# Optimization experiments

Hardware: AMD Instinct MI355X
Metric: run time of the kernel (lower is better)

Reference implementation:

```python
import jax, jax.numpy as jnp
import numpy as np

N_NODES = 100000
N_EDGES = 1600000
IN_C = 64
HID_C = 64
OUT_C = 8


def _glorot(key, shape):
    fan_in, fan_out = shape
    lim = (6.0 / (fan_in + fan_out)) ** 0.5
    return jax.random.uniform(key, shape, jnp.float32, -lim, lim)


def setup_inputs() -> dict:
    key = jax.random.key(0)
    ks = jax.random.split(key, 16)
    inp = {
        "x": jax.random.normal(ks[0], (N_NODES, IN_C), jnp.float32),
        "edge_index": jax.random.randint(ks[1], (2, N_EDGES), 0, N_NODES, jnp.int64),
        "edge_attr": jax.random.normal(ks[2], (N_EDGES, 1), jnp.float32),
        # GIN MLP params: layer i uses Linear(in,h) -> ReLU -> Linear(h,h)
        "l0_w1": _glorot(ks[3], (IN_C, HID_C)), "l0_b1": jnp.zeros((HID_C,), jnp.float32),
        "l0_w2": _glorot(ks[4], (HID_C, HID_C)), "l0_b2": jnp.zeros((HID_C,), jnp.float32),
        "l1_w1": _glorot(ks[5], (HID_C, HID_C)), "l1_b1": jnp.zeros((HID_C,), jnp.float32),
        "l1_w2": _glorot(ks[6], (HID_C, HID_C)), "l1_b2": jnp.zeros((HID_C,), jnp.float32),
        # last layer maps hidden -> out (reduce_dims is None)
        "l2_w1": _glorot(ks[7], (HID_C, OUT_C)), "l2_b1": jnp.zeros((OUT_C,), jnp.float32),
        "l2_w2": _glorot(ks[8], (OUT_C, OUT_C)), "l2_b2": jnp.zeros((OUT_C,), jnp.float32),
    }
    return inp


def _gin_layer(x, src, dst, w1, b1, w2, b2):
    # GINConv with eps=0: out_i = MLP(x_i + sum_{j->i} x_j)
    agg = jax.ops.segment_sum(x[src], dst, num_segments=N_NODES)  # [N, C]
    h = x + agg
    h = jax.nn.relu(h @ w1 + b1)
    return h @ w2 + b2


def reference(x, edge_index, edge_attr,
              l0_w1, l0_b1, l0_w2, l0_b2,
              l1_w1, l1_b1, l1_w2, l1_b2,
              l2_w1, l2_b1, l2_w2, l2_b2):
    src, dst = edge_index[0], edge_index[1]
    # dropout is identity in eval mode
    h = _gin_layer(x, src, dst, l0_w1, l0_b1, l0_w2, l0_b2)
    h = jax.nn.relu(h)
    h = _gin_layer(h, src, dst, l1_w1, l1_b1, l1_w2, l1_b2)
    h = jax.nn.relu(h)
    h = _gin_layer(h, src, dst, l2_w1, l2_b1, l2_w2, l2_b2)  # no relu on last (reduce_dims None)
    return jax.nn.log_softmax(h, axis=-1)
```

## Files before the change

### kernel.cpp

```cpp
#include <hip/hip_runtime.h>
#include <math.h>

#define N_NODES 100000
#define N_EDGES 1600000
#define C 64
#define OUTC 8
#define NBUCK 256
#define BRANGE 391
#define BCAP 7200
#define CNT_PAD 64
#define BUCK_CHUNK 4096

__device__ __forceinline__ float bflo(unsigned u) { return __uint_as_float(u << 16); }
__device__ __forceinline__ float bfhi(unsigned u) { return __uint_as_float(u & 0xFFFF0000u); }
__device__ __forceinline__ unsigned short f2bf(float f) {
    unsigned b = __float_as_uint(f);
    b += 0x7FFFu + ((b >> 16) & 1u);
    return (unsigned short)(b >> 16);
}

__global__ __launch_bounds__(256) void bucket_k(const int* __restrict__ src, const int* __restrict__ dst,
                                                int* cntp, uint2* __restrict__ ebuf, int ne) {
    __shared__ int lcnt[NBUCK], lbase[NBUCK], lcur[NBUCK];
    int t = threadIdx.x;
    if (t < NBUCK) { lcnt[t] = 0; lcur[t] = 0; }
    __syncthreads();
    int base = blockIdx.x * BUCK_CHUNK;
#pragma unroll
    for (int i = 0; i < BUCK_CHUNK / 256; i++) {
        int e = base + i * 256 + t;
        if (e < ne) {
            int d = __builtin_nontemporal_load(dst + e);
            atomicAdd(&lcnt[d / BRANGE], 1);
        }
    }
    __syncthreads();
    if (t < NBUCK) lbase[t] = lcnt[t] ? atomicAdd(&cntp[t * CNT_PAD], lcnt[t]) : 0;
    __syncthreads();
#pragma unroll
    for (int i = 0; i < BUCK_CHUNK / 256; i++) {
        int e = base + i * 256 + t;
        if (e < ne) {
            int d = __builtin_nontemporal_load(dst + e);
            int s = __builtin_nontemporal_load(src + e);
            int r = d / BRANGE;
            int pos = lbase[r] + atomicAdd(&lcur[r], 1);
            if (pos < BCAP) ebuf[(size_t)r * BCAP + pos] = make_uint2((unsigned)s, (unsigned)d);
        }
    }
}

__global__ __launch_bounds__(512) void fill4_k(const int* __restrict__ cntp, const uint2* __restrict__ ebuf,
                                               int* __restrict__ rowptr, int* __restrict__ ssrc) {
    __shared__ int lcnt[BRANGE];
    __shared__ int sm[512];
    __shared__ int lcur[BRANGE];
    __shared__ int cbuf[NBUCK];
    __shared__ int bbase;
    int b = blockIdx.x;
    int lo = b * BRANGE;
    int span = N_NODES - lo; if (span > BRANGE) span = BRANGE; if (span < 0) span = 0;
    int t = threadIdx.x;
    if (t < BRANGE) lcnt[t] = 0;
    if (t < NBUCK) cbuf[t] = cntp[t * CNT_PAD];
    __syncthreads();
    if (t == 0) {
        int s = 0;
        for (int i = 0; i < b; i++) s += cbuf[i];
        bbase = s;
    }
    int cnt = cbuf[b];
    if (cnt > BCAP) cnt = BCAP;
    const uint2* buf = ebuf + (size_t)b * BCAP;
    for (int i = t; i < cnt; i += 512) {
        uint2 ed = buf[i];
        atomicAdd(&lcnt[(int)ed.y - lo], 1);
    }
    __syncthreads();
    int v = (t < BRANGE) ? lcnt[t] : 0;
    sm[t] = v;
    __syncthreads();
    for (int off = 1; off < 512; off <<= 1) {
        int u = (t >= off) ? sm[t - off] : 0;
        __syncthreads();
        sm[t] += u;
        __syncthreads();
    }
    int ex = bbase + sm[t] - v;
    if (t < span) { rowptr[lo + t] = ex; lcur[t] = ex; }
    if (b == NBUCK - 1 && t == 0) rowptr[N_NODES] = N_EDGES;
    __syncthreads();
    for (int i = t; i < cnt; i += 512) {
        uint2 ed = buf[i];
        int p = atomicAdd(&lcur[(int)ed.y - lo], 1);
        ssrc[p] = (int)ed.x;
    }
}

__global__ __launch_bounds__(256) void conv_bf16_k(const float* __restrict__ in, unsigned short* __restrict__ outb, int nElem) {
    int i = blockIdx.x * 256 + threadIdx.x;
    int stride = gridDim.x * 256;
    for (int e = i * 4; e < nElem; e += stride * 4) {
        float4 v = *(const float4*)(in + e);
        ushort4 o;
        o.x = f2bf(v.x); o.y = f2bf(v.y); o.z = f2bf(v.z); o.w = f2bf(v.w);
        *(ushort4*)(outb + e) = o;
    }
}

__global__ __launch_bounds__(256) void gather_bf16_k(const unsigned short* __restrict__ featb,
                                                     const int* __restrict__ rowptr,
                                                     const int* __restrict__ ssrc,
                                                     float* __restrict__ tout, int n) {
    const uint2* feat2 = (const uint2*)featb;
    int lane = threadIdx.x & 63;
    int slot = lane >> 4;
    int chg  = lane & 15;
    int wid = blockIdx.x * 4 + (threadIdx.x >> 6);
    if (wid >= n) return;
    int beg = rowptr[wid], end = rowptr[wid + 1];
    float ax = 0.f, ay = 0.f, az = 0.f, aw = 0.f;
    if (slot == 0) {
        uint2 v = feat2[(size_t)wid * 16 + chg];
        ax = bflo(v.x); ay = bfhi(v.x); az = bflo(v.y); aw = bfhi(v.y);
    }
    int e = beg;
    for (; e + 8 <= end; e += 8) {
        int iA = ssrc[e + slot];
        int iB = ssrc[e + 4 + slot];
        uint2 vA = feat2[(size_t)iA * 16 + chg];
        uint2 vB = feat2[(size_t)iB * 16 + chg];
        ax += bflo(vA.x) + bflo(vB.x);
        ay += bfhi(vA.x) + bfhi(vB.x);
        az += bflo(vA.y) + bflo(vB.y);
        aw += bfhi(vA.y) + bfhi(vB.y);
    }
    for (; e < end; e += 4) {
        int myE = e + slot;
        if (myE < end) {
            int i = ssrc[myE];
            uint2 v = feat2[(size_t)i * 16 + chg];
            ax += bflo(v.x); ay += bfhi(v.x); az += bflo(v.y); aw += bfhi(v.y);
        }
    }
    ax += __shfl_xor(ax, 16, 64); ay += __shfl_xor(ay, 16, 64);
    az += __shfl_xor(az, 16, 64); aw += __shfl_xor(aw, 16, 64);
    ax += __shfl_xor(ax, 32, 64); ay += __shfl_xor(ay, 32, 64);
    az += __shfl_xor(az, 32, 64); aw += __shfl_xor(aw, 32, 64);
    if (slot == 0) ((float4*)tout)[(size_t)wid * 16 + chg] = make_float4(ax, ay, az, aw);
}

__global__ __launch_bounds__(256) void fused_final_bf16_k(const unsigned short* __restrict__ featb,
                                                          const int* __restrict__ rowptr,
                                                          const int* __restrict__ ssrc,
                                                          float* __restrict__ out,
                                                          const float* __restrict__ W1, const float* __restrict__ b1,
                                                          const float* __restrict__ W2, const float* __restrict__ b2,
                                                          int n) {
    const uint2* feat2 = (const uint2*)featb;
    int lane = threadIdx.x & 63;
    int slot = lane >> 4;
    int chg  = lane & 15;
    int j = lane & 7;
    int g = lane >> 3;
    float w1r[8], w2r[8];
#pragma unroll
    for (int i = 0; i < 8; i++) w1r[i] = W1[(g * 8 + i) * OUTC + j];
#pragma unroll
    for (int i = 0; i < 8; i++) w2r[i] = W2[i * OUTC + j];
    float b1j = b1[j], b2j = b2[j];
    int wid = blockIdx.x * 4 + (threadIdx.x >> 6);
    if (wid >= n) return;
    int beg = rowptr[wid], end = rowptr[wid + 1];
    float ax = 0.f, ay = 0.f, az = 0.f, aw = 0.f;
    if (slot == 0) {
        uint2 v = feat2[(size_t)wid * 16 + chg];
        ax = bflo(v.x); ay = bfhi(v.x); az = bflo(v.y); aw = bfhi(v.y);
    }
    int e = beg;
    for (; e + 8 <= end; e += 8) {
        int iA = ssrc[e + slot];
        int iB = ssrc[e + 4 + slot];
        uint2 vA = feat2[(size_t)iA * 16 + chg];
        uint2 vB = feat2[(size_t)iB * 16 + chg];
        ax += bflo(vA.x) + bflo(vB.x);
        ay += bfhi(vA.x) + bfhi(vB.x);
        az += bflo(vA.y) + bflo(vB.y);
        aw += bfhi(vA.y) + bfhi(vB.y);
    }
    for (; e < end; e += 4) {
        int myE = e + slot;
        if (myE < end) {
            int i = ssrc[myE];
            uint2 v = feat2[(size_t)i * 16 + chg];
            ax += bflo(v.x); ay += bfhi(v.x); az += bflo(v.y); aw += bfhi(v.y);
        }
    }
    ax += __shfl_xor(ax, 16, 64); ay += __shfl_xor(ay, 16, 64);
    az += __shfl_xor(az, 16, 64); aw += __shfl_xor(aw, 16, 64);
    ax += __shfl_xor(ax, 32, 64); ay += __shfl_xor(ay, 32, 64);
    az += __shfl_xor(az, 32, 64); aw += __shfl_xor(aw, 32, 64);
    float h = 0.f;
#pragma unroll
    for (int i = 0; i < 8; i++) {
        float compv = (i & 3) == 0 ? ax : (i & 3) == 1 ? ay : (i & 3) == 2 ? az : aw;
        float tm = __shfl(compv, g * 2 + (i >> 2), 64);
        h = fmaf(tm, w1r[i], h);
    }
    h += __shfl_xor(h, 8, 64);
    h += __shfl_xor(h, 16, 64);
    h += __shfl_xor(h, 32, 64);
    h = fmaxf(h + b1j, 0.f);
    float y = b2j;
#pragma unroll
    for (int k = 0; k < 8; k++) {
        float hk = __shfl(h, (lane & ~7) + k, 64);
        y = fmaf(hk, w2r[k], y);
    }
    float m = y;
    m = fmaxf(m, __shfl_xor(m, 1, 64));
    m = fmaxf(m, __shfl_xor(m, 2, 64));
    m = fmaxf(m, __shfl_xor(m, 4, 64));
    float ex = expf(y - m);
    float ssum = ex;
    ssum += __shfl_xor(ssum, 1, 64);
    ssum += __shfl_xor(ssum, 2, 64);
    ssum += __shfl_xor(ssum, 4, 64);
    float res = (y - m) - logf(ssum);
    if (lane < 8) out[(size_t)wid * OUTC + lane] = res;
}

__global__ __launch_bounds__(256) void mlp_gemm_k(const float* __restrict__ tin,
                                                  unsigned short* __restrict__ zoutb,
                                                  const float* __restrict__ W1, const float* __restrict__ b1,
                                                  const float* __restrict__ W2, const float* __restrict__ b2,
                                                  int relu_out) {
    __shared__ float Tl[64][64];
    __shared__ float W1l[64][64];
    __shared__ float W2l[64][64];
    int t = threadIdx.x;
    int nbase = blockIdx.x * 64;
    {
        const float4* w1v = (const float4*)W1; const float4* w2v = (const float4*)W2;
        float4* w1d = (float4*)&W1l[0][0];     float4* w2d = (float4*)&W2l[0][0];
#pragma unroll
        for (int i = 0; i < 4; i++) { w1d[t + 256 * i] = w1v[t + 256 * i]; w2d[t + 256 * i] = w2v[t + 256 * i]; }
    }
    {
        int n = t >> 2, c0 = (t & 3) * 16;
        int gn = nbase + n;
        float4 r[4];
        if (gn < N_NODES) {
#pragma unroll
            for (int i = 0; i < 4; i++) r[i] = *(const float4*)&tin[(size_t)gn * 64 + c0 + 4 * i];
        } else {
#pragma unroll
            for (int i = 0; i < 4; i++) r[i] = make_float4(0.f, 0.f, 0.f, 0.f);
        }
#pragma unroll
        for (int i = 0; i < 4; i++) {
            Tl[c0 + 4 * i + 0][n] = r[i].x; Tl[c0 + 4 * i + 1][n] = r[i].y;
            Tl[c0 + 4 * i + 2][n] = r[i].z; Tl[c0 + 4 * i + 3][n] = r[i].w;
        }
    }
    __syncthreads();
    int tn = t & 15, tc = t >> 4;
    float b1v[4], b2v[4];
#pragma unroll
    for (int i = 0; i < 4; i++) { b1v[i] = b1[4 * tc + i]; b2v[i] = b2[4 * tc + i]; }
    float acc[4][4];
#pragma unroll
    for (int i = 0; i < 4; i++)
#pragma unroll
        for (int j = 0; j < 4; j++) acc[i][j] = 0.f;
#pragma unroll 8
    for (int k = 0; k < 64; k++) {
        float4 tv = *(const float4*)&Tl[k][4 * tn];
        float4 wv = *(const float4*)&W1l[k][4 * tc];
        acc[0][0] = fmaf(wv.x, tv.x, acc[0][0]); acc[0][1] = fmaf(wv.x, tv.y, acc[0][1]);
        acc[0][2] = fmaf(wv.x, tv.z, acc[0][2]); acc[0][3] = fmaf(wv.x, tv.w, acc[0][3]);
        acc[1][0] = fmaf(wv.y, tv.x, acc[1][0]); acc[1][1] = fmaf(wv.y, tv.y, acc[1][1]);
        acc[1][2] = fmaf(wv.y, tv.z, acc[1][2]); acc[1][3] = fmaf(wv.y, tv.w, acc[1][3]);
        acc[2][0] = fmaf(wv.z, tv.x, acc[2][0]); acc[2][1] = fmaf(wv.z, tv.y, acc[2][1]);
        acc[2][2] = fmaf(wv.z, tv.z, acc[2][2]); acc[2][3] = fmaf(wv.z, tv.w, acc[2][3]);
        acc[3][0] = fmaf(wv.w, tv.x, acc[3][0]); acc[3][1] = fmaf(wv.w, tv.y, acc[3][1]);
        acc[3][2] = fmaf(wv.w, tv.z, acc[3][2]); acc[3][3] = fmaf(wv.w, tv.w, acc[3][3]);
    }
    __syncthreads();
#pragma unroll
    for (int i = 0; i < 4; i++) {
        float4 hv;
        hv.x = fmaxf(acc[i][0] + b1v[i], 0.f); hv.y = fmaxf(acc[i][1] + b1v[i], 0.f);
        hv.z = fmaxf(acc[i][2] + b1v[i], 0.f); hv.w = fmaxf(acc[i][3] + b1v[i], 0.f);
        *(float4*)&Tl[4 * tc + i][4 * tn] = hv;
    }
#pragma unroll
    for (int i = 0; i < 4; i++)
#pragma unroll
        for (int j = 0; j < 4; j++) acc[i][j] = 0.f;
    __syncthreads();
#pragma unroll 8
    for (int k = 0; k < 64; k++) {
        float4 tv = *(const float4*)&Tl[k][4 * tn];
        float4 wv = *(const float4*)&W2l[k][4 * tc];
        acc[0][0] = fmaf(wv.x, tv.x, acc[0][0]); acc[0][1] = fmaf(wv.x, tv.y, acc[0][1]);
        acc[0][2] = fmaf(wv.x, tv.z, acc[0][2]); acc[0][3] = fmaf(wv.x, tv.w, acc[0][3]);
        acc[1][0] = fmaf(wv.y, tv.x, acc[1][0]); acc[1][1] = fmaf(wv.y, tv.y, acc[1][1]);
        acc[1][2] = fmaf(wv.y, tv.z, acc[1][2]); acc[1][3] = fmaf(wv.y, tv.w, acc[1][3]);
        acc[2][0] = fmaf(wv.z, tv.x, acc[2][0]); acc[2][1] = fmaf(wv.z, tv.y, acc[2][1]);
        acc[2][2] = fmaf(wv.z, tv.z, acc[2][2]); acc[2][3] = fmaf(wv.z, tv.w, acc[2][3]);
        acc[3][0] = fmaf(wv.w, tv.x, acc[3][0]); acc[3][1] = fmaf(wv.w, tv.y, acc[3][1]);
        acc[3][2] = fmaf(wv.w, tv.z, acc[3][2]); acc[3][3] = fmaf(wv.w, tv.w, acc[3][3]);
    }
    unsigned short* ob = (unsigned short*)&W1l[0][0];
#pragma unroll
    for (int j = 0; j < 4; j++) {
        float y0 = acc[0][j] + b2v[0], y1 = acc[1][j] + b2v[1];
        float y2 = acc[2][j] + b2v[2], y3 = acc[3][j] + b2v[3];
        if (relu_out) {
            y0 = fmaxf(y0, 0.f); y1 = fmaxf(y1, 0.f);
            y2 = fmaxf(y2, 0.f); y3 = fmaxf(y3, 0.f);
        }
        uint2 p;
        p.x = (unsigned)f2bf(y0) | ((unsigned)f2bf(y1) << 16);
        p.y = (unsigned)f2bf(y2) | ((unsigned)f2bf(y3) << 16);
        *(uint2*)&ob[(4 * tn + j) * 64 + 4 * tc] = p;
    }
    __syncthreads();
    {
        const uint4* sb = (const uint4*)ob;
        uint4* gb = (uint4*)(zoutb + (size_t)nbase * 64);
        size_t elemBase = (size_t)nbase * 64;
#pragma unroll
        for (int s = 0; s < 2; s++) {
            int idx = 2 * t + s;
            if (elemBase + (size_t)idx * 8 < (size_t)N_NODES * 64) gb[idx] = sb[idx];
        }
    }
}

extern "C" void kernel_launch(void* const* d_in, const int* in_sizes, int n_in,
                              void* d_out, int out_size, void* d_ws, size_t ws_size,
                              hipStream_t stream) {
    const float* x = (const float*)d_in[0];
    const int* ei = (const int*)d_in[1];
    const float* l0w1 = (const float*)d_in[3],  *l0b1 = (const float*)d_in[4];
    const float* l0w2 = (const float*)d_in[5],  *l0b2 = (const float*)d_in[6];
    const float* l1w1 = (const float*)d_in[7],  *l1b1 = (const float*)d_in[8];
    const float* l1w2 = (const float*)d_in[9],  *l1b2 = (const float*)d_in[10];
    const float* l2w1 = (const float*)d_in[11], *l2b1 = (const float*)d_in[12];
    const float* l2w2 = (const float*)d_in[13], *l2b2 = (const float*)d_in[14];
    float* out = (float*)d_out;
    const int* src = ei;
    const int* dst = ei + N_EDGES;

    char* ws = (char*)d_ws;
    size_t off = 0;
    auto carve = [&](size_t bytes) -> void* {
        void* p = ws + off;
        off += (bytes + 255) & ~(size_t)255;
        return p;
    };
    int* cntp   = (int*)carve((size_t)NBUCK * CNT_PAD * 4);
    int* rowptr = (int*)carve((size_t)(N_NODES + 1) * 4);
    int* ssrc   = (int*)carve((size_t)N_EDGES * 4);
    unsigned short* xb = (unsigned short*)carve((size_t)N_NODES * C * 2);
    unsigned short* zb = (unsigned short*)carve((size_t)(N_NODES + 64) * C * 2);
    float* tb   = (float*)carve((size_t)N_NODES * C * 4);
    uint2* ebuf = (uint2*)tb;
    (void)ws_size;

    hipMemsetAsync(cntp, 0, (size_t)NBUCK * CNT_PAD * 4, stream);
    bucket_k<<<(N_EDGES + BUCK_CHUNK - 1) / BUCK_CHUNK, 256, 0, stream>>>(src, dst, cntp, ebuf, N_EDGES);
    fill4_k<<<NBUCK, 512, 0, stream>>>(cntp, ebuf, rowptr, ssrc);

    conv_bf16_k<<<2048, 256, 0, stream>>>(x, xb, N_NODES * C);

    int gblocks = (N_NODES + 3) / 4;
    int mblocks = (N_NODES + 63) / 64;
    gather_bf16_k<<<gblocks, 256, 0, stream>>>(xb, rowptr, ssrc, tb, N_NODES);
    mlp_gemm_k<<<mblocks, 256, 0, stream>>>(tb, zb, l0w1, l0b1, l0w2, l0b2, 1);
    gather_bf16_k<<<gblocks, 256, 0, stream>>>(zb, rowptr, ssrc, tb, N_NODES);
    mlp_gemm_k<<<mblocks, 256, 0, stream>>>(tb, zb, l1w1, l1b1, l1w2, l1b2, 1);
    fused_final_bf16_k<<<gblocks, 256, 0, stream>>>(zb, rowptr, ssrc, out, l2w1, l2b1, l2w2, l2b2, N_NODES);
}
```

Measured before the change: 274.0 us.

## Sort neighbor lists by source range in CSR build and unroll gather loops deeper

The CSR fill kernel now builds a joint histogram keyed by (destination row, source group of 4096 nodes), scans it, and scatters each edge in that order. Within every row the neighbors therefore come out roughly sorted by source id, which should give the feature gathers better cache locality. The gather kernels also unroll to 16 edges per iteration with four independent loads in flight per lane. The cost is a larger shared histogram, a serial 20-element scan per thread, and more registers in the gather kernels.

```diff
diff --git a/kernel.cpp b/kernel.cpp
--- a/kernel.cpp
+++ b/kernel.cpp
@@ -10,6 +10,8 @@
 #define BCAP 7200
 #define CNT_PAD 64
 #define BUCK_CHUNK 4096
+#define SGRP 25
+#define HSZ (BRANGE * SGRP)
 
 __device__ __forceinline__ float bflo(unsigned u) { return __uint_as_float(u << 16); }
 __device__ __forceinline__ float bfhi(unsigned u) { return __uint_as_float(u & 0xFFFF0000u); }
@@ -50,18 +52,17 @@
     }
 }
 
-__global__ __launch_bounds__(512) void fill4_k(const int* __restrict__ cntp, const uint2* __restrict__ ebuf,
+__global__ __launch_bounds__(512) void fill5_k(const int* __restrict__ cntp, const uint2* __restrict__ ebuf,
                                                int* __restrict__ rowptr, int* __restrict__ ssrc) {
-    __shared__ int lcnt[BRANGE];
-    __shared__ int sm[512];
-    __shared__ int lcur[BRANGE];
+    __shared__ int H[HSZ];
+    __shared__ int part[512];
     __shared__ int cbuf[NBUCK];
     __shared__ int bbase;
     int b = blockIdx.x;
     int lo = b * BRANGE;
     int span = N_NODES - lo; if (span > BRANGE) span = BRANGE; if (span < 0) span = 0;
     int t = threadIdx.x;
-    if (t < BRANGE) lcnt[t] = 0;
+    for (int i = t; i < HSZ; i += 512) H[i] = 0;
     if (t < NBUCK) cbuf[t] = cntp[t * CNT_PAD];
     __syncthreads();
     if (t == 0) {
@@ -74,25 +75,34 @@
     const uint2* buf = ebuf + (size_t)b * BCAP;
     for (int i = t; i < cnt; i += 512) {
         uint2 ed = buf[i];
-        atomicAdd(&lcnt[(int)ed.y - lo], 1);
-    }
-    __syncthreads();
-    int v = (t < BRANGE) ? lcnt[t] : 0;
-    sm[t] = v;
+        atomicAdd(&H[((int)ed.y - lo) * SGRP + ((int)ed.x >> 12)], 1);
+    }
+    __syncthreads();
+    const int IPT = 20;
+    int base = t * IPT, s = 0;
+#pragma unroll
+    for (int i = 0; i < IPT; i++) { int idx = base + i; if (idx < HSZ) s += H[idx]; }
+    part[t] = s;
     __syncthreads();
     for (int off = 1; off < 512; off <<= 1) {
-        int u = (t >= off) ? sm[t - off] : 0;
+        int u = (t >= off) ? part[t - off] : 0;
         __syncthreads();
-        sm[t] += u;
+        part[t] += u;
         __syncthreads();
     }
-    int ex = bbase + sm[t] - v;
-    if (t < span) { rowptr[lo + t] = ex; lcur[t] = ex; }
+    int run = part[t] - s;
+#pragma unroll
+    for (int i = 0; i < IPT; i++) {
+        int idx = base + i;
+        if (idx < HSZ) { int v = H[idx]; H[idx] = run; run += v; }
+    }
+    __syncthreads();
+    if (t < span) rowptr[lo + t] = bbase + H[t * SGRP];
     if (b == NBUCK - 1 && t == 0) rowptr[N_NODES] = N_EDGES;
     __syncthreads();
     for (int i = t; i < cnt; i += 512) {
         uint2 ed = buf[i];
-        int p = atomicAdd(&lcur[(int)ed.y - lo], 1);
+        int p = bbase + atomicAdd(&H[((int)ed.y - lo) * SGRP + ((int)ed.x >> 12)], 1);
         ssrc[p] = (int)ed.x;
     }
 }
@@ -125,23 +135,29 @@
         ax = bflo(v.x); ay = bfhi(v.x); az = bflo(v.y); aw = bfhi(v.y);
     }
     int e = beg;
-    for (; e + 8 <= end; e += 8) {
-        int iA = ssrc[e + slot];
-        int iB = ssrc[e + 4 + slot];
-        uint2 vA = feat2[(size_t)iA * 16 + chg];
-        uint2 vB = feat2[(size_t)iB * 16 + chg];
-        ax += bflo(vA.x) + bflo(vB.x);
-        ay += bfhi(vA.x) + bfhi(vB.x);
-        az += bflo(vA.y) + bflo(vB.y);
-        aw += bfhi(vA.y) + bfhi(vB.y);
-    }
-    for (; e < end; e += 4) {
-        int myE = e + slot;
-        if (myE < end) {
-            int i = ssrc[myE];
-            uint2 v = feat2[(size_t)i * 16 + chg];
-            ax += bflo(v.x); ay += bfhi(v.x); az += bflo(v.y); aw += bfhi(v.y);
-        }
+    for (; e + 16 <= end; e += 16) {
+        int i0 = ssrc[e + slot];
+        int i1 = ssrc[e + 4 + slot];
+        int i2 = ssrc[e + 8 + slot];
+        int i3 = ssrc[e + 12 + slot];
+        uint2 v0 = feat2[(size_t)i0 * 16 + chg];
+        uint2 v1 = feat2[(size_t)i1 * 16 + chg];
+        uint2 v2 = feat2[(size_t)i2 * 16 + chg];
+        uint2 v3 = feat2[(size_t)i3 * 16 + chg];
+        ax += (bflo(v0.x) + bflo(v1.x)) + (bflo(v2.x) + bflo(v3.x));
+        ay += (bfhi(v0.x) + bfhi(v1.x)) + (bfhi(v2.x) + bfhi(v3.x));
+        az += (bflo(v0.y) + bflo(v1.y)) + (bflo(v2.y) + bflo(v3.y));
+        aw += (bfhi(v0.y) + bfhi(v1.y)) + (bfhi(v2.y) + bfhi(v3.y));
+    }
+    for (; e + 4 <= end; e += 4) {
+        int i = ssrc[e + slot];
+        uint2 v = feat2[(size_t)i * 16 + chg];
+        ax += bflo(v.x); ay += bfhi(v.x); az += bflo(v.y); aw += bfhi(v.y);
+    }
+    if (e + slot < end) {
+        int i = ssrc[e + slot];
+        uint2 v = feat2[(size_t)i * 16 + chg];
+        ax += bflo(v.x); ay += bfhi(v.x); az += bflo(v.y); aw += bfhi(v.y);
     }
     ax += __shfl_xor(ax, 16, 64); ay += __shfl_xor(ay, 16, 64);
     az += __shfl_xor(az, 16, 64); aw += __shfl_xor(aw, 16, 64);
@@ -178,23 +194,29 @@
         ax = bflo(v.x); ay = bfhi(v.x); az = bflo(v.y); aw = bfhi(v.y);
     }
     int e = beg;
-    for (; e + 8 <= end; e += 8) {
-        int iA = ssrc[e + slot];
-        int iB = ssrc[e + 4 + slot];
-        uint2 vA = feat2[(size_t)iA * 16 + chg];
-        uint2 vB = feat2[(size_t)iB * 16 + chg];
-        ax += bflo(vA.x) + bflo(vB.x);
-        ay += bfhi(vA.x) + bfhi(vB.x);
-        az += bflo(vA.y) + bflo(vB.y);
-        aw += bfhi(vA.y) + bfhi(vB.y);
-    }
-    for (; e < end; e += 4) {
-        int myE = e + slot;
-        if (myE < end) {
-            int i = ssrc[myE];
-            uint2 v = feat2[(size_t)i * 16 + chg];
-            ax += bflo(v.x); ay += bfhi(v.x); az += bflo(v.y); aw += bfhi(v.y);
-        }
+    for (; e + 16 <= end; e += 16) {
+        int i0 = ssrc[e + slot];
+        int i1 = ssrc[e + 4 + slot];
+        int i2 = ssrc[e + 8 + slot];
+        int i3 = ssrc[e + 12 + slot];
+        uint2 v0 = feat2[(size_t)i0 * 16 + chg];
+        uint2 v1 = feat2[(size_t)i1 * 16 + chg];
+        uint2 v2 = feat2[(size_t)i2 * 16 + chg];
+        uint2 v3 = feat2[(size_t)i3 * 16 + chg];
+        ax += (bflo(v0.x) + bflo(v1.x)) + (bflo(v2.x) + bflo(v3.x));
+        ay += (bfhi(v0.x) + bfhi(v1.x)) + (bfhi(v2.x) + bfhi(v3.x));
+        az += (bflo(v0.y) + bflo(v1.y)) + (bflo(v2.y) + bflo(v3.y));
+        aw += (bfhi(v0.y) + bfhi(v1.y)) + (bfhi(v2.y) + bfhi(v3.y));
+    }
+    for (; e + 4 <= end; e += 4) {
+        int i = ssrc[e + slot];
+        uint2 v = feat2[(size_t)i * 16 + chg];
+        ax += bflo(v.x); ay += bfhi(v.x); az += bflo(v.y); aw += bfhi(v.y);
+    }
+    if (e + slot < end) {
+        int i = ssrc[e + slot];
+        uint2 v = feat2[(size_t)i * 16 + chg];
+        ax += bflo(v.x); ay += bfhi(v.x); az += bflo(v.y); aw += bfhi(v.y);
     }
     ax += __shfl_xor(ax, 16, 64); ay += __shfl_xor(ay, 16, 64);
     az += __shfl_xor(az, 16, 64); aw += __shfl_xor(aw, 16, 64);
@@ -370,9 +392,9 @@
     uint2* ebuf = (uint2*)tb;
     (void)ws_size;
 
-    hipMemsetAsync(cntp, 0, (size_t)NBUCK * CNT_PAD * 4, stream);
+    (void)hipMemsetAsync(cntp, 0, (size_t)NBUCK * CNT_PAD * 4, stream);
     bucket_k<<<(N_EDGES + BUCK_CHUNK - 1) / BUCK_CHUNK, 256, 0, stream>>>(src, dst, cntp, ebuf, N_EDGES);
-    fill4_k<<<NBUCK, 512, 0, stream>>>(cntp, ebuf, rowptr, ssrc);
+    fill5_k<<<NBUCK, 512, 0, stream>>>(cntp, ebuf, rowptr, ssrc);
 
     conv_bf16_k<<<2048, 256, 0, stream>>>(x, xb, N_NODES * C);
 
```

Result: no change. 276.2 us (+0.8%).
